# Kernel tuning notes

Measured on AMD Instinct MI355X. Metric: run time of the kernel, lower is better.

## Reference

```python
import jax, jax.numpy as jnp
import numpy as np

B, S, D, H = 4, 2048, 1024, 16
HD = D // H  # head dim = 64


def setup_inputs() -> dict:
    key = jax.random.key(0)
    ks = jax.random.split(key, 12)
    s = 1.0 / np.sqrt(D)
    return {
        "query": jax.random.normal(ks[0], (B, S, D), jnp.float32),
        "key": jax.random.normal(ks[1], (B, S, D), jnp.float32),
        "value": jax.random.normal(ks[2], (B, S, D), jnp.float32),
        "attention_mask": jnp.zeros((B, S, S), jnp.float32),
        "Wq": jax.random.normal(ks[3], (D, D), jnp.float32) * s,
        "bq": jax.random.normal(ks[4], (D,), jnp.float32) * s,
        "Wk": jax.random.normal(ks[5], (D, D), jnp.float32) * s,
        "bk": jax.random.normal(ks[6], (D,), jnp.float32) * s,
        "Wv": jax.random.normal(ks[7], (D, D), jnp.float32) * s,
        "bv": jax.random.normal(ks[8], (D,), jnp.float32) * s,
        "Wo": jax.random.normal(ks[9], (D, D), jnp.float32) * s,
        "bo": jax.random.normal(ks[10], (D,), jnp.float32) * s,
    }


def reference(query, key, value, attention_mask, Wq, bq, Wk, bk, Wv, bv, Wo, bo):
    # projections (torch Linear: x @ W.T + b)
    q = query @ Wq.T + bq
    k = key @ Wk.T + bk
    v = value @ Wv.T + bv
    # split heads: [B, S, D] -> [B, H, S, HD]
    split = lambda x: x.reshape(B, S, H, HD).transpose(0, 2, 1, 3)
    q, k, v = split(q), split(k), split(v)
    # scores: [B, H, Sq, Sk], scaled and masked (mask broadcast over heads)
    scores = jnp.einsum("bhqd,bhkd->bhqk", q, k) / jnp.sqrt(jnp.asarray(HD, q.dtype))
    scores = scores + attention_mask[:, None, :, :]
    probs = jax.nn.softmax(scores, axis=-1)
    out = jnp.einsum("bhqk,bhkd->bhqd", probs, v)
    # concat heads: [B, H, S, HD] -> [B, S, D]
    out = out.transpose(0, 2, 1, 3).reshape(B, S, D)
    return out @ Wo.T + bo
```

## Files before the change

### kernel.cpp

```cpp
#include <hip/hip_runtime.h>
#include <hip/hip_bf16.h>


typedef float f32x4 __attribute__((ext_vector_type(4)));
typedef float f32x16 __attribute__((ext_vector_type(16)));
typedef short bf16x8 __attribute__((ext_vector_type(8)));

#define LOG2E 1.4426950408889634f

__device__ __forceinline__ void gload_lds16(const void* g, void* l) {
  __builtin_amdgcn_global_load_lds((const __attribute__((address_space(1))) void*)g,
                                   (__attribute__((address_space(3))) void*)l,
                                   16, 0, 0);
}

__device__ __forceinline__ float fast_exp2(float x) {
#if __has_builtin(__builtin_amdgcn_exp2f)
  return __builtin_amdgcn_exp2f(x);
#else
  return exp2f(x);
#endif
}

__device__ __forceinline__ unsigned bf16bits(float x) {
  __hip_bfloat16 h = __float2bfloat16(x);
  return (unsigned)*(unsigned short*)&h;
}

__device__ __forceinline__ void pl32swap(unsigned& a, unsigned& b, int hi) {
#if __has_builtin(__builtin_amdgcn_permlane32_swap)
  typedef unsigned uint2v __attribute__((ext_vector_type(2)));
  uint2v r = __builtin_amdgcn_permlane32_swap(a, b, false, false);
  a = r[0];
  b = r[1];
#else
  unsigned ax = __shfl_xor((int)a, 32);
  unsigned bx = __shfl_xor((int)b, 32);
  unsigned na = hi ? bx : a;
  unsigned nb = hi ? b : ax;
  a = na;
  b = nb;
#endif
}

__device__ __forceinline__ bf16x8 lds_read_swz(const __hip_bfloat16* base, int row, int colByte) {
  int off = row * 128 + (colByte ^ ((row & 7) << 4));
  return *(const bf16x8*)((const char*)base + off);
}

__global__ __launch_bounds__(256) void cvt3(const float* __restrict__ s0,
                                            const float* __restrict__ s1,
                                            const float* __restrict__ s2,
                                            __hip_bfloat16* __restrict__ d0,
                                            __hip_bfloat16* __restrict__ d1,
                                            __hip_bfloat16* __restrict__ d2, int n) {
  const float* s = blockIdx.z == 0 ? s0 : (blockIdx.z == 1 ? s1 : s2);
  __hip_bfloat16* d = blockIdx.z == 0 ? d0 : (blockIdx.z == 1 ? d1 : d2);
  int i = (blockIdx.x * 256 + threadIdx.x) * 8;
  if (i + 8 <= n) {
    float4 x = *(const float4*)(s + i);
    float4 y = *(const float4*)(s + i + 4);
    bf16x8 v;
    __hip_bfloat16* hv = (__hip_bfloat16*)&v;
    hv[0] = __float2bfloat16(x.x); hv[1] = __float2bfloat16(x.y);
    hv[2] = __float2bfloat16(x.z); hv[3] = __float2bfloat16(x.w);
    hv[4] = __float2bfloat16(y.x); hv[5] = __float2bfloat16(y.y);
    hv[6] = __float2bfloat16(y.z); hv[7] = __float2bfloat16(y.w);
    *(bf16x8*)(d + i) = v;
  }
}

__global__ __launch_bounds__(256) void cvt4(const float* __restrict__ s0,
                                            const float* __restrict__ s1,
                                            const float* __restrict__ s2,
                                            const float* __restrict__ s3,
                                            __hip_bfloat16* __restrict__ d0,
                                            __hip_bfloat16* __restrict__ d1,
                                            __hip_bfloat16* __restrict__ d2,
                                            __hip_bfloat16* __restrict__ d3, int n) {
  const float* s = blockIdx.z == 0 ? s0 : (blockIdx.z == 1 ? s1 : (blockIdx.z == 2 ? s2 : s3));
  __hip_bfloat16* d = blockIdx.z == 0 ? d0 : (blockIdx.z == 1 ? d1 : (blockIdx.z == 2 ? d2 : d3));
  int i = (blockIdx.x * 256 + threadIdx.x) * 8;
  if (i + 8 <= n) {
    float4 x = *(const float4*)(s + i);
    float4 y = *(const float4*)(s + i + 4);
    bf16x8 v;
    __hip_bfloat16* hv = (__hip_bfloat16*)&v;
    hv[0] = __float2bfloat16(x.x); hv[1] = __float2bfloat16(x.y);
    hv[2] = __float2bfloat16(x.z); hv[3] = __float2bfloat16(x.w);
    hv[4] = __float2bfloat16(y.x); hv[5] = __float2bfloat16(y.y);
    hv[6] = __float2bfloat16(y.z); hv[7] = __float2bfloat16(y.w);
    *(bf16x8*)(d + i) = v;
  }
}

template <int MODE>
__global__ __launch_bounds__(256) void gemm_nt(const __hip_bfloat16* __restrict__ A,
                                               const __hip_bfloat16* __restrict__ W,
                                               const float* __restrict__ bias,
                                               void* __restrict__ out, float scale) {
  extern __shared__ char smem[];
  __hip_bfloat16(*As)[64] = (__hip_bfloat16(*)[64])smem;
  __hip_bfloat16(*Bs)[64] = (__hip_bfloat16(*)[64])(smem + 128 * 64 * 2);

  const int t = threadIdx.x;
  const int w = t >> 6, l = t & 63;
  const int wm = w >> 1, wn = w & 1;
  const int rowbase = blockIdx.y * 128;
  const int colbase = blockIdx.x * 128;
  const int lr = l & 15, lg = l >> 4;
  const int srow = l >> 3, schunk = (l & 7) * 8;

  f32x4 acc[4][4];
#pragma unroll
  for (int m = 0; m < 4; m++)
#pragma unroll
    for (int n = 0; n < 4; n++) acc[m][n] = {0.f, 0.f, 0.f, 0.f};

  for (int kt = 0; kt < 16; ++kt) {
    const int k0 = kt * 64;
#pragma unroll
    for (int i = 0; i < 4; i++) {
      int r = w * 32 + i * 8;
      gload_lds16(A + (size_t)(rowbase + r + srow) * 1024 + k0 + schunk, &As[r][0]);
      gload_lds16(W + (size_t)(colbase + r + srow) * 1024 + k0 + schunk, &Bs[r][0]);
    }
    __syncthreads();
#pragma unroll
    for (int kk = 0; kk < 2; kk++) {
      bf16x8 a[4], b[4];
#pragma unroll
      for (int m = 0; m < 4; m++) a[m] = *(const bf16x8*)&As[wm * 64 + m * 16 + lr][kk * 32 + lg * 8];
#pragma unroll
      for (int n = 0; n < 4; n++) b[n] = *(const bf16x8*)&Bs[wn * 64 + n * 16 + lr][kk * 32 + lg * 8];
#pragma unroll
      for (int m = 0; m < 4; m++)
#pragma unroll
        for (int n = 0; n < 4; n++)
          acc[m][n] = __builtin_amdgcn_mfma_f32_16x16x32_bf16(a[m], b[n], acc[m][n], 0, 0, 0);
    }
    __syncthreads();
  }

  if (MODE == 0 || MODE == 2) {
#pragma unroll
    for (int m = 0; m < 4; m++) {
#pragma unroll
      for (int r = 0; r < 4; r++) {
        int gi = rowbase + wm * 64 + m * 16 + lg * 4 + r;
#pragma unroll
        for (int n = 0; n < 4; n++) {
          int gj = colbase + wn * 64 + n * 16 + lr;
          float v = (acc[m][n][r] + bias[gj]) * scale;
          if (MODE == 0)
            ((__hip_bfloat16*)out)[(size_t)gi * 1024 + gj] = __float2bfloat16(v);
          else
            ((float*)out)[(size_t)gi * 1024 + gj] = v;
        }
      }
    }
  } else {
    __hip_bfloat16* Ts = (__hip_bfloat16*)smem;
#pragma unroll
    for (int m = 0; m < 4; m++)
#pragma unroll
      for (int r = 0; r < 4; r++) {
        int rr = wm * 64 + m * 16 + lg * 4 + r;
#pragma unroll
        for (int n = 0; n < 4; n++) {
          int c = wn * 64 + n * 16 + lr;
          Ts[rr * 130 + c] = __float2bfloat16(acc[m][n][r] + bias[colbase + c]);
        }
      }
    __syncthreads();
    int d = t >> 1, s0 = (t & 1) * 64;
    int gd = colbase + d;
    int h = gd >> 6, hd = gd & 63;
    int gs = rowbase + s0;
    int b = gs >> 11, sl = gs & 2047;
    __hip_bfloat16* dst = (__hip_bfloat16*)out + ((size_t)(b * 16 + h) * 64 + hd) * 2048 + sl;
#pragma unroll
    for (int c8 = 0; c8 < 8; c8++) {
      bf16x8 v;
#pragma unroll
      for (int j = 0; j < 8; j++)
        ((unsigned short*)&v)[j] = ((const unsigned short*)Ts)[(s0 + c8 * 8 + j) * 130 + d];
      *(bf16x8*)(dst + c8 * 8) = v;
    }
  }
}

__global__ __launch_bounds__(256, 4) void attn(const __hip_bfloat16* __restrict__ Q,
                                               const __hip_bfloat16* __restrict__ K,
                                               const __hip_bfloat16* __restrict__ Vt,
                                               const float* __restrict__ mask,
                                               __hip_bfloat16* __restrict__ O) {
  __shared__ __hip_bfloat16 Ks[2][64][64];
  __shared__ __hip_bfloat16 Vs[2][64][64];

  const int t = threadIdx.x, w = t >> 6, l = t & 63;
  const int l31 = l & 31, hi = l >> 5;
  int lin = blockIdx.y * 16 + blockIdx.x;
  lin = (lin & 7) * 128 + (lin >> 3);
  const int qt = lin & 15, bh = lin >> 4;
  const int b = bh >> 4, h = bh & 15;
  const int q0 = qt * 128 + w * 32;
  const size_t bS = (size_t)b * 2048;
  const int srow = l >> 3;
  const int swchunk = ((l & 7) * 8) ^ (srow << 3);

#define STAGE(dbuf, ktile)                                                             \
  do {                                                                                 \
    int kb_ = (ktile) * 64;                                                            \
    _Pragma("unroll") for (int i_ = 0; i_ < 2; i_++) {                                 \
      int r_ = w * 16 + i_ * 8;                                                        \
      gload_lds16(K + (bS + kb_ + r_ + srow) * 1024 + h * 64 + swchunk,                \
                  &Ks[dbuf][r_][0]);                                                   \
      gload_lds16(Vt + ((size_t)bh * 64 + r_ + srow) * 2048 + kb_ + swchunk,           \
                  &Vs[dbuf][r_][0]);                                                   \
    }                                                                                  \
  } while (0)

  bf16x8 qf[4];
#pragma unroll
  for (int c = 0; c < 4; c++)
    qf[c] = *(const bf16x8*)(Q + (bS + q0 + l31) * 1024 + h * 64 + c * 16 + hi * 8);

  f32x16 acco[2];
#pragma unroll
  for (int i = 0; i < 16; i++) { acco[0][i] = 0.f; acco[1][i] = 0.f; }
  float m2 = -1e30f, lsum = 0.f;

  STAGE(0, 0);
  __syncthreads();
  int cur = 0;

  const float* mrow = mask + (bS + q0 + l31) * 2048;

  for (int kt = 0; kt < 32; ++kt) {
    const int kb = kt * 64;
    if (kt < 31) STAGE(cur ^ 1, kt + 1);

    f32x16 sc[2];
#pragma unroll
    for (int ks = 0; ks < 2; ks++)
#pragma unroll
      for (int g = 0; g < 4; g++) {
        float4 tmp = *(const float4*)(mrow + kb + ks * 32 + g * 8 + hi * 4);
        sc[ks][g * 4 + 0] = tmp.x * LOG2E; sc[ks][g * 4 + 1] = tmp.y * LOG2E;
        sc[ks][g * 4 + 2] = tmp.z * LOG2E; sc[ks][g * 4 + 3] = tmp.w * LOG2E;
      }

    __builtin_amdgcn_s_setprio(1);
#pragma unroll
    for (int c = 0; c < 4; c++) {
      bf16x8 ka0 = lds_read_swz(&Ks[cur][0][0], l31, c * 32 + hi * 16);
      sc[0] = __builtin_amdgcn_mfma_f32_32x32x16_bf16(ka0, qf[c], sc[0], 0, 0, 0);
      bf16x8 ka1 = lds_read_swz(&Ks[cur][0][0], 32 + l31, c * 32 + hi * 16);
      sc[1] = __builtin_amdgcn_mfma_f32_32x32x16_bf16(ka1, qf[c], sc[1], 0, 0, 0);
    }
    __builtin_amdgcn_s_setprio(0);

    float mx[16];
#pragma unroll
    for (int r = 0; r < 16; r++) mx[r] = fmaxf(sc[0][r], sc[1][r]);
#pragma unroll
    for (int s = 8; s >= 1; s >>= 1)
#pragma unroll
      for (int r = 0; r < s; r++) mx[r] = fmaxf(mx[r], mx[r + s]);
    float tmax = fmaxf(mx[0], __shfl_xor(mx[0], 32));

    if (__any(tmax > m2 + 8.0f)) {
      float mn = fmaxf(m2, tmax);
      float rs = fast_exp2(m2 - mn);
      m2 = mn;
      lsum *= rs;
#pragma unroll
      for (int r = 0; r < 16; r++) {
        float rsr = __shfl(rs, (r & 3) + 8 * (r >> 2) + 4 * hi);
        acco[0][r] *= rsr;
        acco[1][r] *= rsr;
      }
    }

    float ts0 = 0.f, ts1 = 0.f;
    unsigned pk[2][4][2];
#pragma unroll
    for (int ks = 0; ks < 2; ks++)
#pragma unroll
      for (int g = 0; g < 4; g++)
#pragma unroll
        for (int s = 0; s < 2; s++) {
          float p0 = fast_exp2(sc[ks][g * 4 + s * 2] - m2);
          float p1 = fast_exp2(sc[ks][g * 4 + s * 2 + 1] - m2);
          ts0 += p0;
          ts1 += p1;
          pk[ks][g][s] = (bf16bits(p1) << 16) | bf16bits(p0);
        }
    float tsum = ts0 + ts1;
    tsum += __shfl_xor(tsum, 32);
    lsum += tsum;

    __builtin_amdgcn_s_setprio(1);
#pragma unroll
    for (int ks = 0; ks < 2; ks++) {
#pragma unroll
      for (int c16 = 0; c16 < 2; c16++) {
        unsigned x0 = pk[ks][2 * c16][0], y0 = pk[ks][2 * c16 + 1][0];
        unsigned x1 = pk[ks][2 * c16][1], y1 = pk[ks][2 * c16 + 1][1];
        pl32swap(x0, y0, hi);
        pl32swap(x1, y1, hi);
        bf16x8 pa;
        ((unsigned*)&pa)[0] = x0; ((unsigned*)&pa)[1] = x1;
        ((unsigned*)&pa)[2] = y0; ((unsigned*)&pa)[3] = y1;
#pragma unroll
        for (int ds = 0; ds < 2; ds++) {
          bf16x8 vb = lds_read_swz(&Vs[cur][0][0], ds * 32 + l31, ks * 64 + c16 * 32 + hi * 16);
          acco[ds] = __builtin_amdgcn_mfma_f32_32x32x16_bf16(pa, vb, acco[ds], 0, 0, 0);
        }
      }
    }
    __builtin_amdgcn_s_setprio(0);
    __syncthreads();
    cur ^= 1;
  }
#undef STAGE

  float inv = 1.0f / lsum;
#pragma unroll
  for (int r = 0; r < 16; r++) {
    float invr = __shfl(inv, (r & 3) + 8 * (r >> 2) + 4 * hi);
    int q = q0 + (r & 3) + 8 * (r >> 2) + 4 * hi;
#pragma unroll
    for (int ds = 0; ds < 2; ds++)
      O[(bS + q) * 1024 + h * 64 + ds * 32 + l31] = __float2bfloat16(acco[ds][r] * invr);
  }
}

extern "C" void kernel_launch(void* const* d_in, const int* in_sizes, int n_in,
                              void* d_out, int out_size, void* d_ws, size_t ws_size,
                              hipStream_t stream) {
  const float* q = (const float*)d_in[0];
  const float* k = (const float*)d_in[1];
  const float* v = (const float*)d_in[2];
  const float* msk = (const float*)d_in[3];
  const float* Wq = (const float*)d_in[4];
  const float* bq = (const float*)d_in[5];
  const float* Wk = (const float*)d_in[6];
  const float* bk = (const float*)d_in[7];
  const float* Wv = (const float*)d_in[8];
  const float* bv = (const float*)d_in[9];
  const float* Wo = (const float*)d_in[10];
  const float* bo = (const float*)d_in[11];

  char* ws = (char*)d_ws;
  __hip_bfloat16* qin = (__hip_bfloat16*)(ws);
  __hip_bfloat16* kin = (__hip_bfloat16*)(ws + (16u << 20));
  __hip_bfloat16* vin = (__hip_bfloat16*)(ws + (32u << 20));
  __hip_bfloat16* wqb = (__hip_bfloat16*)(ws + (48u << 20));
  __hip_bfloat16* wkb = (__hip_bfloat16*)(ws + (50u << 20));
  __hip_bfloat16* wvb = (__hip_bfloat16*)(ws + (52u << 20));
  __hip_bfloat16* wob = (__hip_bfloat16*)(ws + (54u << 20));
  __hip_bfloat16* vT  = (__hip_bfloat16*)(ws + (56u << 20));
  __hip_bfloat16* kp  = vin;
  __hip_bfloat16* qp  = kin;
  __hip_bfloat16* oat = qin;

  dim3 blk(256);
  size_t smem = 33280;
  const float qscale = 0.125f * LOG2E;

  cvt3<<<dim3(4096, 1, 3), blk, 0, stream>>>(q, k, v, qin, kin, vin, 8388608);
  cvt4<<<dim3(512, 1, 4), blk, 0, stream>>>(Wq, Wk, Wv, Wo, wqb, wkb, wvb, wob, 1048576);
  gemm_nt<1><<<dim3(8, 64), blk, smem, stream>>>(vin, wvb, bv, vT, 1.0f);
  gemm_nt<0><<<dim3(8, 64), blk, smem, stream>>>(kin, wkb, bk, kp, 1.0f);
  gemm_nt<0><<<dim3(8, 64), blk, smem, stream>>>(qin, wqb, bq, qp, qscale);
  attn<<<dim3(16, 64), blk, 0, stream>>>(qp, kp, vT, msk, oat);
  gemm_nt<2><<<dim3(8, 64), blk, smem, stream>>>(oat, wob, bo, (float*)d_out, 1.0f);
}
```

Measured before the change: 313.8 us.

## Convert attention mask to bf16 once and prefetch mask tiles into registers

Adds a pre-pass that converts the fp32 attention mask to bf16 with the LOG2E factor folded in. The attention kernel then reads the narrower mask, halving mask traffic, since the mask is re-read for every head. The mask loads for the next key tile are now issued into registers during the current iteration, hiding their latency behind the MFMA work. The costs are an extra conversion kernel, 32 MB of extra workspace, and reduced mask precision. The bf16 path only runs when the workspace is large enough; otherwise the fp32 path with prefetch is used.

Measured after the change: 323.9 us. 1.03x slower.

```diff
diff --git a/kernel.cpp b/kernel.cpp
--- a/kernel.cpp
+++ b/kernel.cpp
@@ -5,6 +5,7 @@
 typedef float f32x4 __attribute__((ext_vector_type(4)));
 typedef float f32x16 __attribute__((ext_vector_type(16)));
 typedef short bf16x8 __attribute__((ext_vector_type(8)));
+typedef short short4v __attribute__((ext_vector_type(4)));
 
 #define LOG2E 1.4426950408889634f
 
@@ -94,6 +95,20 @@
   }
 }
 
+__global__ __launch_bounds__(256) void cvtmask(const float* __restrict__ s,
+                                               __hip_bfloat16* __restrict__ d) {
+  int i = (blockIdx.x * 256 + threadIdx.x) * 8;
+  float4 x = *(const float4*)(s + i);
+  float4 y = *(const float4*)(s + i + 4);
+  bf16x8 v;
+  __hip_bfloat16* hv = (__hip_bfloat16*)&v;
+  hv[0] = __float2bfloat16(x.x * LOG2E); hv[1] = __float2bfloat16(x.y * LOG2E);
+  hv[2] = __float2bfloat16(x.z * LOG2E); hv[3] = __float2bfloat16(x.w * LOG2E);
+  hv[4] = __float2bfloat16(y.x * LOG2E); hv[5] = __float2bfloat16(y.y * LOG2E);
+  hv[6] = __float2bfloat16(y.z * LOG2E); hv[7] = __float2bfloat16(y.w * LOG2E);
+  *(bf16x8*)(d + i) = v;
+}
+
 template <int MODE>
 __global__ __launch_bounds__(256) void gemm_nt(const __hip_bfloat16* __restrict__ A,
                                                const __hip_bfloat16* __restrict__ W,
@@ -190,10 +205,11 @@
   }
 }
 
+template <int MBF>
 __global__ __launch_bounds__(256, 4) void attn(const __hip_bfloat16* __restrict__ Q,
                                                const __hip_bfloat16* __restrict__ K,
                                                const __hip_bfloat16* __restrict__ Vt,
-                                               const float* __restrict__ mask,
+                                               const void* __restrict__ mask,
                                                __hip_bfloat16* __restrict__ O) {
   __shared__ __hip_bfloat16 Ks[2][64][64];
   __shared__ __hip_bfloat16 Vs[2][64][64];
@@ -235,21 +251,47 @@
   __syncthreads();
   int cur = 0;
 
-  const float* mrow = mask + (bS + q0 + l31) * 2048;
+  const unsigned short* mrowh = (const unsigned short*)mask + (bS + q0 + l31) * 2048;
+  const float* mrowf = (const float*)mask + (bS + q0 + l31) * 2048;
+
+  short4v mh[8];
+  f32x4 mf[8];
+#pragma unroll
+  for (int ks = 0; ks < 2; ks++)
+#pragma unroll
+    for (int g = 0; g < 4; g++) {
+      int idx = ks * 32 + g * 8 + hi * 4;
+      if (MBF) mh[ks * 4 + g] = *(const short4v*)(mrowh + idx);
+      else     mf[ks * 4 + g] = *(const f32x4*)(mrowf + idx);
+    }
 
   for (int kt = 0; kt < 32; ++kt) {
-    const int kb = kt * 64;
     if (kt < 31) STAGE(cur ^ 1, kt + 1);
 
     f32x16 sc[2];
 #pragma unroll
     for (int ks = 0; ks < 2; ks++)
 #pragma unroll
-      for (int g = 0; g < 4; g++) {
-        float4 tmp = *(const float4*)(mrow + kb + ks * 32 + g * 8 + hi * 4);
-        sc[ks][g * 4 + 0] = tmp.x * LOG2E; sc[ks][g * 4 + 1] = tmp.y * LOG2E;
-        sc[ks][g * 4 + 2] = tmp.z * LOG2E; sc[ks][g * 4 + 3] = tmp.w * LOG2E;
-      }
+      for (int g = 0; g < 4; g++)
+#pragma unroll
+        for (int j = 0; j < 4; j++) {
+          if (MBF)
+            sc[ks][g * 4 + j] = __uint_as_float(((unsigned)(unsigned short)mh[ks * 4 + g][j]) << 16);
+          else
+            sc[ks][g * 4 + j] = mf[ks * 4 + g][j] * LOG2E;
+        }
+
+    if (kt < 31) {
+      int nb = (kt + 1) * 64;
+#pragma unroll
+      for (int ks = 0; ks < 2; ks++)
+#pragma unroll
+        for (int g = 0; g < 4; g++) {
+          int idx = nb + ks * 32 + g * 8 + hi * 4;
+          if (MBF) mh[ks * 4 + g] = *(const short4v*)(mrowh + idx);
+          else     mf[ks * 4 + g] = *(const f32x4*)(mrowf + idx);
+        }
+    }
 
     __builtin_amdgcn_s_setprio(1);
 #pragma unroll
@@ -362,19 +404,27 @@
   __hip_bfloat16* wvb = (__hip_bfloat16*)(ws + (52u << 20));
   __hip_bfloat16* wob = (__hip_bfloat16*)(ws + (54u << 20));
   __hip_bfloat16* vT  = (__hip_bfloat16*)(ws + (56u << 20));
+  __hip_bfloat16* maskbf = (__hip_bfloat16*)(ws + (72u << 20));
   __hip_bfloat16* kp  = vin;
   __hip_bfloat16* qp  = kin;
   __hip_bfloat16* oat = qin;
 
+  const bool use_bf16_mask = ws_size >= ((72ull << 20) + (32ull << 20));
+
   dim3 blk(256);
   size_t smem = 33280;
   const float qscale = 0.125f * LOG2E;
 
   cvt3<<<dim3(4096, 1, 3), blk, 0, stream>>>(q, k, v, qin, kin, vin, 8388608);
   cvt4<<<dim3(512, 1, 4), blk, 0, stream>>>(Wq, Wk, Wv, Wo, wqb, wkb, wvb, wob, 1048576);
+  if (use_bf16_mask)
+    cvtmask<<<dim3(8192), blk, 0, stream>>>(msk, maskbf);
   gemm_nt<1><<<dim3(8, 64), blk, smem, stream>>>(vin, wvb, bv, vT, 1.0f);
   gemm_nt<0><<<dim3(8, 64), blk, smem, stream>>>(kin, wkb, bk, kp, 1.0f);
   gemm_nt<0><<<dim3(8, 64), blk, smem, stream>>>(qin, wqb, bq, qp, qscale);
-  attn<<<dim3(16, 64), blk, 0, stream>>>(qp, kp, vT, msk, oat);
+  if (use_bf16_mask)
+    attn<1><<<dim3(16, 64), blk, 0, stream>>>(qp, kp, vT, maskbf, oat);
+  else
+    attn<0><<<dim3(16, 64), blk, 0, stream>>>(qp, kp, vT, msk, oat);
   gemm_nt<2><<<dim3(8, 64), blk, smem, stream>>>(oat, wob, bo, (float*)d_out, 1.0f);
 }
```
